# Performance work log

Measured on AMD Instinct MI355X. Metric: run time of the kernel, lower is better.

Reference implementation:

```python
import jax, jax.numpy as jnp
from jax import lax
import numpy as np

T, B, I = 512, 64, 1024
L, H = 2, 1024

def setup_inputs() -> dict:
    key = jax.random.key(0)
    k1, k2, k3 = jax.random.split(key, 3)
    scale = 1.0 / np.sqrt(H)
    return {
        "x": jax.random.normal(k1, (T, B, I), dtype=jnp.float32),
        "w_ih": jax.random.normal(k2, (L, 4 * H, I), dtype=jnp.float32) * scale,
        "w_hh": jax.random.normal(k3, (L, 4 * H, H), dtype=jnp.float32) * scale,
        "b_ih": jnp.zeros((L, 4 * H), dtype=jnp.float32),
        "b_hh": jnp.zeros((L, 4 * H), dtype=jnp.float32),
    }

def _lstm_layer(seq, wi, wh, b):
    # seq: [T, B, D]; wi: [4H, D]; wh: [4H, H]; b: [4H]
    Bsz = seq.shape[1]
    Hh = wh.shape[1]
    # precompute input projection for all timesteps (one big GEMM)
    xin = jnp.einsum('tbd,gd->tbg', seq, wi) + b  # [T, B, 4H]
    def step(carry, xt):
        h, c = carry
        gates = xt + h @ wh.T  # [B, 4H]
        i, f, g, o = jnp.split(gates, 4, axis=1)
        c = jax.nn.sigmoid(f) * c + jax.nn.sigmoid(i) * jnp.tanh(g)
        h = jax.nn.sigmoid(o) * jnp.tanh(c)
        return (h, c), h
    h0 = jnp.zeros((Bsz, Hh), seq.dtype)
    c0 = jnp.zeros((Bsz, Hh), seq.dtype)
    (hn, cn), out = lax.scan(step, (h0, c0), xin)
    return out, hn, cn

def reference(x, w_ih, w_hh, b_ih, b_hh):
    seq = x
    h_n, c_n = [], []
    for l in range(w_hh.shape[0]):
        seq, hn, cn = _lstm_layer(seq, w_ih[l], w_hh[l], b_ih[l] + b_hh[l])
        h_n.append(hn)
        c_n.append(cn)
    return seq, jnp.stack(h_n, 0), jnp.stack(c_n, 0)
```

## Files before the change

kernel.cpp:

```cpp
#include <hip/hip_runtime.h>
#include <cstddef>
#include <cstdint>

#define T_LEN   512
#define BATCH   64
#define IN_DIM  1024
#define HID     1024
#define GATES   4096
#define NLAYERS 2
#define BH      (BATCH * HID)
#define RBLK    256

typedef __bf16 bf16;
typedef __bf16 bf16x8 __attribute__((ext_vector_type(8)));
typedef float  f32x4  __attribute__((ext_vector_type(4)));

__global__ __launch_bounds__(256) void cvt_bf16(const float* __restrict__ in,
                                                bf16* __restrict__ out, int n4) {
    int i = blockIdx.x * blockDim.x + threadIdx.x;
    if (i >= n4) return;
    float4 v = ((const float4*)in)[i];
    bf16 o[4] = {(bf16)v.x, (bf16)v.y, (bf16)v.z, (bf16)v.w};
    *(uint2*)(out + 4 * (size_t)i) = *(uint2*)o;
}

__global__ __launch_bounds__(256) void lstm_layer(
    const bf16*  __restrict__ wi,
    const bf16*  __restrict__ wh,
    const float* __restrict__ bih,
    const float* __restrict__ bhh,
    const bf16*  __restrict__ xbf,
    bf16*        __restrict__ hseq,
    float*       __restrict__ outf,
    float*       __restrict__ hf32,
    float*       __restrict__ cbuf,
    unsigned*    __restrict__ bar)
{
    __shared__ bf16  Bi[16 * 1032];
    __shared__ bf16  Bh[16 * 1032];
    __shared__ float sg[4 * 272];

    const int bk   = blockIdx.x;
    const int j0   = bk * 4;
    const int tid  = threadIdx.x;
    const int lane = tid & 63;
    const int wv   = tid >> 6;
    const int m0   = wv * 16;
    const int quad = lane >> 4;
    const int l16  = lane & 15;

    unsigned* flags   = bar;
    unsigned* release = bar + 384;

    #pragma unroll
    for (int i = 0; i < 8; ++i) {
        int flat = i * 256 + tid;
        int row  = flat >> 7;
        int k16  = flat & 127;
        int grr  = (row >> 2) * 1024 + j0 + (row & 3);
        *(uint4*)&Bi[row * 1032 + k16 * 8] =
            *(const uint4*)(wi + (size_t)grr * IN_DIM + k16 * 8);
        *(uint4*)&Bh[row * 1032 + k16 * 8] =
            *(const uint4*)(wh + (size_t)grr * HID + k16 * 8);
    }

    const int cb = m0 + l16;
    const int cu = j0 + quad;
    float c = 0.f;

    const int gr = (l16 >> 2) * 1024 + j0 + (l16 & 3);
    const int bb = m0 + quad * 4;
    const float bias = bih[gr] + bhh[gr];

    __syncthreads();

    const bf16*  bibase = &Bi[l16 * 1032 + quad * 8];
    const bf16*  bhbase = &Bh[l16 * 1032 + quad * 8];
    const size_t arow   = (size_t)(m0 + l16) * HID + quad * 8;

    f32x4 acc0, acc1, acc2, acc3;
    {
        const bf16* xp = xbf + arow;
        acc0 = {bias, bias, bias, bias};
        acc1 = {0.f, 0.f, 0.f, 0.f};
        acc2 = {0.f, 0.f, 0.f, 0.f};
        acc3 = {0.f, 0.f, 0.f, 0.f};
        #pragma unroll
        for (int q = 0; q < 8; ++q) {
            const int k0 = q * 32;
            acc0 = __builtin_amdgcn_mfma_f32_16x16x32_bf16(
                *(const bf16x8*)(xp + k0),       *(const bf16x8*)(bibase + k0),       acc0, 0, 0, 0);
            acc1 = __builtin_amdgcn_mfma_f32_16x16x32_bf16(
                *(const bf16x8*)(xp + 256 + k0), *(const bf16x8*)(bibase + 256 + k0), acc1, 0, 0, 0);
            acc2 = __builtin_amdgcn_mfma_f32_16x16x32_bf16(
                *(const bf16x8*)(xp + 512 + k0), *(const bf16x8*)(bibase + 512 + k0), acc2, 0, 0, 0);
            acc3 = __builtin_amdgcn_mfma_f32_16x16x32_bf16(
                *(const bf16x8*)(xp + 768 + k0), *(const bf16x8*)(bibase + 768 + k0), acc3, 0, 0, 0);
        }
    }

    for (int tt = 0; tt < T_LEN; ++tt) {
        if (tt > 0) {
            const unsigned ep = (unsigned)tt;
            if (tid == 0) {
                unsigned guard = 0;
                while (__hip_atomic_load(release, __ATOMIC_RELAXED,
                                         __HIP_MEMORY_SCOPE_AGENT) < ep) {
                    __builtin_amdgcn_s_sleep(1);
                    if (++guard > (1u << 16)) break;
                }
            }
            __syncthreads();
            const bf16* hp = hseq + (size_t)(tt - 1) * BH + arow;
            #pragma unroll
            for (int q = 0; q < 8; ++q) {
                const int k0 = q * 32;
                acc0 = __builtin_amdgcn_mfma_f32_16x16x32_bf16(
                    *(const bf16x8*)(hp + k0),       *(const bf16x8*)(bhbase + k0),       acc0, 0, 0, 0);
                acc1 = __builtin_amdgcn_mfma_f32_16x16x32_bf16(
                    *(const bf16x8*)(hp + 256 + k0), *(const bf16x8*)(bhbase + 256 + k0), acc1, 0, 0, 0);
                acc2 = __builtin_amdgcn_mfma_f32_16x16x32_bf16(
                    *(const bf16x8*)(hp + 512 + k0), *(const bf16x8*)(bhbase + 512 + k0), acc2, 0, 0, 0);
                acc3 = __builtin_amdgcn_mfma_f32_16x16x32_bf16(
                    *(const bf16x8*)(hp + 768 + k0), *(const bf16x8*)(bhbase + 768 + k0), acc3, 0, 0, 0);
            }
        }

        f32x4 g4 = (acc0 + acc1) + (acc2 + acc3);

        #pragma unroll
        for (int r = 0; r < 4; ++r)
            sg[wv * 272 + (quad * 4 + r) * 17 + l16] = g4[r];
        const float* gp = &sg[wv * 272 + l16 * 17];
        float gi = gp[quad], gf = gp[4 + quad], gg = gp[8 + quad], go = gp[12 + quad];

        float si  = 1.f / (1.f + expf(-gi));
        float sf_ = 1.f / (1.f + expf(-gf));
        float so  = 1.f / (1.f + expf(-go));
        float cv  = sf_ * c + si * tanhf(gg);
        float hv  = so * tanhf(cv);
        c = cv;

        const size_t idx = (size_t)cb * HID + cu;
        float hvn = __shfl_xor(hv, 16);
        if ((quad & 1) == 0) {
            bf16 hb  = (bf16)hv;
            bf16 hbn = (bf16)hvn;
            unsigned pk = (unsigned)__builtin_bit_cast(unsigned short, hb) |
                          ((unsigned)__builtin_bit_cast(unsigned short, hbn) << 16);
            __hip_atomic_store((unsigned*)(hseq + (size_t)tt * BH + idx), pk,
                               __ATOMIC_RELAXED, __HIP_MEMORY_SCOPE_AGENT);
        }
        if (outf) outf[(size_t)tt * BH + idx] = hv;
        if (tt == T_LEN - 1) hf32[idx] = hv;

        if (tt != T_LEN - 1) {
            const unsigned ep = (unsigned)(tt + 1);
            asm volatile("s_waitcnt vmcnt(0)" ::: "memory");
            __syncthreads();
            if (tid == 0)
                __hip_atomic_store(flags + bk, ep,
                                   __ATOMIC_RELAXED, __HIP_MEMORY_SCOPE_AGENT);

            const bf16* xp = xbf + (size_t)(tt + 1) * BH + arow;
            acc0 = {bias, bias, bias, bias};
            acc1 = {0.f, 0.f, 0.f, 0.f};
            acc2 = {0.f, 0.f, 0.f, 0.f};
            acc3 = {0.f, 0.f, 0.f, 0.f};
            #pragma unroll
            for (int q = 0; q < 8; ++q) {
                const int k0 = q * 32;
                acc0 = __builtin_amdgcn_mfma_f32_16x16x32_bf16(
                    *(const bf16x8*)(xp + k0),       *(const bf16x8*)(bibase + k0),       acc0, 0, 0, 0);
                acc1 = __builtin_amdgcn_mfma_f32_16x16x32_bf16(
                    *(const bf16x8*)(xp + 256 + k0), *(const bf16x8*)(bibase + 256 + k0), acc1, 0, 0, 0);
                acc2 = __builtin_amdgcn_mfma_f32_16x16x32_bf16(
                    *(const bf16x8*)(xp + 512 + k0), *(const bf16x8*)(bibase + 512 + k0), acc2, 0, 0, 0);
                acc3 = __builtin_amdgcn_mfma_f32_16x16x32_bf16(
                    *(const bf16x8*)(xp + 768 + k0), *(const bf16x8*)(bibase + 768 + k0), acc3, 0, 0, 0);
            }

            if (bk == 0 && tid < 64) {
                unsigned guard = 0;
                for (;;) {
                    unsigned f0 = __hip_atomic_load(flags + tid,
                                   __ATOMIC_RELAXED, __HIP_MEMORY_SCOPE_AGENT);
                    unsigned f1 = __hip_atomic_load(flags + 64 + tid,
                                   __ATOMIC_RELAXED, __HIP_MEMORY_SCOPE_AGENT);
                    unsigned f2 = __hip_atomic_load(flags + 128 + tid,
                                   __ATOMIC_RELAXED, __HIP_MEMORY_SCOPE_AGENT);
                    unsigned f3 = __hip_atomic_load(flags + 192 + tid,
                                   __ATOMIC_RELAXED, __HIP_MEMORY_SCOPE_AGENT);
                    if (__all(f0 >= ep && f1 >= ep && f2 >= ep && f3 >= ep)) break;
                    __builtin_amdgcn_s_sleep(1);
                    if (++guard > (1u << 16)) break;
                }
                if (tid == 0)
                    __hip_atomic_store(release, ep,
                                       __ATOMIC_RELAXED, __HIP_MEMORY_SCOPE_AGENT);
            }
        }
    }

    cbuf[(size_t)cb * HID + cu] = c;
}

extern "C" void kernel_launch(void* const* d_in, const int* in_sizes, int n_in,
                              void* d_out, int out_size, void* d_ws, size_t ws_size,
                              hipStream_t stream) {
    const float* x    = (const float*)d_in[0];
    const float* w_ih = (const float*)d_in[1];
    const float* w_hh = (const float*)d_in[2];
    const float* b_ih = (const float*)d_in[3];
    const float* b_hh = (const float*)d_in[4];
    float* out = (float*)d_out;

    float* cbuf = (float*)d_ws;
    float* hf32 = cbuf + (size_t)BATCH * HID;
    bf16* seq1bf = (bf16*)(hf32 + (size_t)BATCH * HID);
    bf16* xh0    = seq1bf + (size_t)T_LEN * BATCH * HID;
    bf16* wibf   = xh0 + (size_t)T_LEN * BATCH * HID;
    bf16* whbf   = wibf + (size_t)GATES * IN_DIM;
    unsigned* bar = (unsigned*)(whbf + (size_t)GATES * HID);

    const size_t seqE = (size_t)T_LEN * BATCH * HID;
    const size_t BHs  = (size_t)BATCH * HID;

    cvt_bf16<<<(int)(seqE / 4 + 255) / 256, 256, 0, stream>>>(x, xh0, (int)(seqE / 4));

    for (int l = 0; l < NLAYERS; ++l) {
        const float* wi = w_ih + (size_t)l * GATES * IN_DIM;
        const float* wh = w_hh + (size_t)l * GATES * HID;
        const float* bi = b_ih + (size_t)l * GATES;
        const float* bh = b_hh + (size_t)l * GATES;

        cvt_bf16<<<(GATES * IN_DIM / 4 + 255) / 256, 256, 0, stream>>>(wi, wibf, GATES * IN_DIM / 4);
        cvt_bf16<<<(GATES * HID / 4 + 255) / 256, 256, 0, stream>>>(wh, whbf, GATES * HID / 4);

        hipMemsetAsync(bar, 0, 512 * sizeof(unsigned), stream);

        const bf16* xin_l = (l == 0) ? xh0 : seq1bf;
        bf16*       hseq  = (l == 0) ? seq1bf : xh0;
        float*      outf  = (l == 1) ? out : nullptr;

        const bf16*  wic = wibf;  const bf16* whc = whbf;
        const float* bic = bi;    const float* bhc = bh;
        float* hfc = hf32;  float* cbc = cbuf;  unsigned* barc = bar;
        void* args[10] = { (void*)&wic, (void*)&whc, (void*)&bic, (void*)&bhc,
                           (void*)&xin_l, (void*)&hseq, (void*)&outf,
                           (void*)&hfc, (void*)&cbc, (void*)&barc };
        hipLaunchCooperativeKernel((void*)lstm_layer, dim3(RBLK), dim3(256),
                                   args, 0, stream);

        hipMemcpyAsync(out + seqE + (size_t)l * BHs, hf32, BHs * sizeof(float),
                       hipMemcpyDeviceToDevice, stream);
        hipMemcpyAsync(out + seqE + (size_t)(NLAYERS + l) * BHs, cbuf, BHs * sizeof(float),
                       hipMemcpyDeviceToDevice, stream);
    }
}
```

Baseline: 10.15 ms.

## Pipeline both LSTM layers in one cooperative kernel with wavefront schedule

Replaces the two sequential per-layer cooperative launches with a single 512-block launch. Blocks 0-255 run layer 0 and blocks 256-511 run layer 1, with layer 1 lagging one timestep and sharing a grid barrier. This targets the serial latency of running 2x512 recurrent steps back to back by overlapping the layers into 513 barrier steps. In exchange, layer-1 steps do the input projection inside the critical path, the barrier now polls 512 flags, and the design depends on 512 blocks being co-resident.

```diff
diff --git a/kernel.cpp b/kernel.cpp
--- a/kernel.cpp
+++ b/kernel.cpp
@@ -9,7 +9,8 @@
 #define GATES   4096
 #define NLAYERS 2
 #define BH      (BATCH * HID)
-#define RBLK    256
+#define LBLK    256
+#define NBLK    512
 
 typedef __bf16 bf16;
 typedef __bf16 bf16x8 __attribute__((ext_vector_type(8)));
@@ -24,16 +25,35 @@
     *(uint2*)(out + 4 * (size_t)i) = *(uint2*)o;
 }
 
-__global__ __launch_bounds__(256) void lstm_layer(
-    const bf16*  __restrict__ wi,
-    const bf16*  __restrict__ wh,
+#define GEMV8(XP, BB)                                                          \
+    _Pragma("unroll")                                                          \
+    for (int q = 0; q < 8; ++q) {                                              \
+        const int k0 = q * 32;                                                 \
+        acc0 = __builtin_amdgcn_mfma_f32_16x16x32_bf16(                        \
+            *(const bf16x8*)((XP) + k0),       *(const bf16x8*)((BB) + k0),       acc0, 0, 0, 0); \
+        acc1 = __builtin_amdgcn_mfma_f32_16x16x32_bf16(                        \
+            *(const bf16x8*)((XP) + 256 + k0), *(const bf16x8*)((BB) + 256 + k0), acc1, 0, 0, 0); \
+        acc2 = __builtin_amdgcn_mfma_f32_16x16x32_bf16(                        \
+            *(const bf16x8*)((XP) + 512 + k0), *(const bf16x8*)((BB) + 512 + k0), acc2, 0, 0, 0); \
+        acc3 = __builtin_amdgcn_mfma_f32_16x16x32_bf16(                        \
+            *(const bf16x8*)((XP) + 768 + k0), *(const bf16x8*)((BB) + 768 + k0), acc3, 0, 0, 0); \
+    }
+
+__global__ __launch_bounds__(256) void lstm_pipe(
+    const bf16*  __restrict__ wi0,
+    const bf16*  __restrict__ wh0,
+    const bf16*  __restrict__ wi1,
+    const bf16*  __restrict__ wh1,
     const float* __restrict__ bih,
     const float* __restrict__ bhh,
     const bf16*  __restrict__ xbf,
-    bf16*        __restrict__ hseq,
+    bf16*        __restrict__ h0seq,
+    bf16*        __restrict__ h1seq,
     float*       __restrict__ outf,
-    float*       __restrict__ hf32,
-    float*       __restrict__ cbuf,
+    float*       __restrict__ hf0,
+    float*       __restrict__ hf1,
+    float*       __restrict__ cb0,
+    float*       __restrict__ cb1,
     unsigned*    __restrict__ bar)
 {
     __shared__ bf16  Bi[16 * 1032];
@@ -41,7 +61,9 @@
     __shared__ float sg[4 * 272];
 
     const int bk   = blockIdx.x;
-    const int j0   = bk * 4;
+    const bool isL1 = (bk >= LBLK);
+    const int lk   = bk & (LBLK - 1);
+    const int j0   = lk * 4;
     const int tid  = threadIdx.x;
     const int lane = tid & 63;
     const int wv   = tid >> 6;
@@ -50,7 +72,14 @@
     const int l16  = lane & 15;
 
     unsigned* flags   = bar;
-    unsigned* release = bar + 384;
+    unsigned* release = bar + 768;
+
+    const bf16* wiL = isL1 ? wi1 : wi0;
+    const bf16* whL = isL1 ? wh1 : wh0;
+    const int   boff = isL1 ? GATES : 0;
+    bf16*       hW  = isL1 ? h1seq : h0seq;
+    float*      hfL = isL1 ? hf1 : hf0;
+    float*      cbL = isL1 ? cb1 : cb0;
 
     #pragma unroll
     for (int i = 0; i < 8; ++i) {
@@ -59,9 +88,9 @@
         int k16  = flat & 127;
         int grr  = (row >> 2) * 1024 + j0 + (row & 3);
         *(uint4*)&Bi[row * 1032 + k16 * 8] =
-            *(const uint4*)(wi + (size_t)grr * IN_DIM + k16 * 8);
+            *(const uint4*)(wiL + (size_t)grr * IN_DIM + k16 * 8);
         *(uint4*)&Bh[row * 1032 + k16 * 8] =
-            *(const uint4*)(wh + (size_t)grr * HID + k16 * 8);
+            *(const uint4*)(whL + (size_t)grr * HID + k16 * 8);
     }
 
     const int cb = m0 + l16;
@@ -69,8 +98,7 @@
     float c = 0.f;
 
     const int gr = (l16 >> 2) * 1024 + j0 + (l16 & 3);
-    const int bb = m0 + quad * 4;
-    const float bias = bih[gr] + bhh[gr];
+    const float bias = bih[boff + gr] + bhh[boff + gr];
 
     __syncthreads();
 
@@ -79,29 +107,18 @@
     const size_t arow   = (size_t)(m0 + l16) * HID + quad * 8;
 
     f32x4 acc0, acc1, acc2, acc3;
-    {
+    if (!isL1) {
         const bf16* xp = xbf + arow;
         acc0 = {bias, bias, bias, bias};
         acc1 = {0.f, 0.f, 0.f, 0.f};
         acc2 = {0.f, 0.f, 0.f, 0.f};
         acc3 = {0.f, 0.f, 0.f, 0.f};
-        #pragma unroll
-        for (int q = 0; q < 8; ++q) {
-            const int k0 = q * 32;
-            acc0 = __builtin_amdgcn_mfma_f32_16x16x32_bf16(
-                *(const bf16x8*)(xp + k0),       *(const bf16x8*)(bibase + k0),       acc0, 0, 0, 0);
-            acc1 = __builtin_amdgcn_mfma_f32_16x16x32_bf16(
-                *(const bf16x8*)(xp + 256 + k0), *(const bf16x8*)(bibase + 256 + k0), acc1, 0, 0, 0);
-            acc2 = __builtin_amdgcn_mfma_f32_16x16x32_bf16(
-                *(const bf16x8*)(xp + 512 + k0), *(const bf16x8*)(bibase + 512 + k0), acc2, 0, 0, 0);
-            acc3 = __builtin_amdgcn_mfma_f32_16x16x32_bf16(
-                *(const bf16x8*)(xp + 768 + k0), *(const bf16x8*)(bibase + 768 + k0), acc3, 0, 0, 0);
-        }
-    }
-
-    for (int tt = 0; tt < T_LEN; ++tt) {
-        if (tt > 0) {
-            const unsigned ep = (unsigned)tt;
+        GEMV8(xp, bibase)
+    }
+
+    for (int s = 0; s < T_LEN + 1; ++s) {
+        if (s > 0) {
+            const unsigned ep = (unsigned)s;
             if (tid == 0) {
                 unsigned guard = 0;
                 while (__hip_atomic_load(release, __ATOMIC_RELAXED,
@@ -111,87 +128,86 @@
                 }
             }
             __syncthreads();
-            const bf16* hp = hseq + (size_t)(tt - 1) * BH + arow;
+        }
+
+        const bool active = isL1 ? (s >= 1) : (s < T_LEN);
+        if (active) {
+            const int t = isL1 ? (s - 1) : s;
+            if (isL1) {
+                const bf16* xp = h0seq + (size_t)t * BH + arow;
+                acc0 = {bias, bias, bias, bias};
+                acc1 = {0.f, 0.f, 0.f, 0.f};
+                acc2 = {0.f, 0.f, 0.f, 0.f};
+                acc3 = {0.f, 0.f, 0.f, 0.f};
+                GEMV8(xp, bibase)
+                if (t > 0) {
+                    const bf16* hp = h1seq + (size_t)(t - 1) * BH + arow;
+                    GEMV8(hp, bhbase)
+                }
+            } else {
+                if (t > 0) {
+                    const bf16* hp = h0seq + (size_t)(t - 1) * BH + arow;
+                    GEMV8(hp, bhbase)
+                }
+            }
+
+            f32x4 g4 = (acc0 + acc1) + (acc2 + acc3);
+
             #pragma unroll
-            for (int q = 0; q < 8; ++q) {
-                const int k0 = q * 32;
-                acc0 = __builtin_amdgcn_mfma_f32_16x16x32_bf16(
-                    *(const bf16x8*)(hp + k0),       *(const bf16x8*)(bhbase + k0),       acc0, 0, 0, 0);
-                acc1 = __builtin_amdgcn_mfma_f32_16x16x32_bf16(
-                    *(const bf16x8*)(hp + 256 + k0), *(const bf16x8*)(bhbase + 256 + k0), acc1, 0, 0, 0);
-                acc2 = __builtin_amdgcn_mfma_f32_16x16x32_bf16(
-                    *(const bf16x8*)(hp + 512 + k0), *(const bf16x8*)(bhbase + 512 + k0), acc2, 0, 0, 0);
-                acc3 = __builtin_amdgcn_mfma_f32_16x16x32_bf16(
-                    *(const bf16x8*)(hp + 768 + k0), *(const bf16x8*)(bhbase + 768 + k0), acc3, 0, 0, 0);
-            }
+            for (int r = 0; r < 4; ++r)
+                sg[wv * 272 + (quad * 4 + r) * 17 + l16] = g4[r];
+            const float* gp = &sg[wv * 272 + l16 * 17];
+            float gi = gp[quad], gf = gp[4 + quad], gg = gp[8 + quad], go = gp[12 + quad];
+
+            float si  = 1.f / (1.f + expf(-gi));
+            float sf_ = 1.f / (1.f + expf(-gf));
+            float so  = 1.f / (1.f + expf(-go));
+            float cv  = sf_ * c + si * tanhf(gg);
+            float hv  = so * tanhf(cv);
+            c = cv;
+
+            const size_t idx = (size_t)cb * HID + cu;
+            float hvn = __shfl_xor(hv, 16);
+            if ((quad & 1) == 0) {
+                bf16 hb  = (bf16)hv;
+                bf16 hbn = (bf16)hvn;
+                unsigned pk = (unsigned)__builtin_bit_cast(unsigned short, hb) |
+                              ((unsigned)__builtin_bit_cast(unsigned short, hbn) << 16);
+                __hip_atomic_store((unsigned*)(hW + (size_t)t * BH + idx), pk,
+                                   __ATOMIC_RELAXED, __HIP_MEMORY_SCOPE_AGENT);
+            }
+            if (isL1) outf[(size_t)t * BH + idx] = hv;
+            if (t == T_LEN - 1) hfL[idx] = hv;
         }
 
-        f32x4 g4 = (acc0 + acc1) + (acc2 + acc3);
-
-        #pragma unroll
-        for (int r = 0; r < 4; ++r)
-            sg[wv * 272 + (quad * 4 + r) * 17 + l16] = g4[r];
-        const float* gp = &sg[wv * 272 + l16 * 17];
-        float gi = gp[quad], gf = gp[4 + quad], gg = gp[8 + quad], go = gp[12 + quad];
-
-        float si  = 1.f / (1.f + expf(-gi));
-        float sf_ = 1.f / (1.f + expf(-gf));
-        float so  = 1.f / (1.f + expf(-go));
-        float cv  = sf_ * c + si * tanhf(gg);
-        float hv  = so * tanhf(cv);
-        c = cv;
-
-        const size_t idx = (size_t)cb * HID + cu;
-        float hvn = __shfl_xor(hv, 16);
-        if ((quad & 1) == 0) {
-            bf16 hb  = (bf16)hv;
-            bf16 hbn = (bf16)hvn;
-            unsigned pk = (unsigned)__builtin_bit_cast(unsigned short, hb) |
-                          ((unsigned)__builtin_bit_cast(unsigned short, hbn) << 16);
-            __hip_atomic_store((unsigned*)(hseq + (size_t)tt * BH + idx), pk,
-                               __ATOMIC_RELAXED, __HIP_MEMORY_SCOPE_AGENT);
-        }
-        if (outf) outf[(size_t)tt * BH + idx] = hv;
-        if (tt == T_LEN - 1) hf32[idx] = hv;
-
-        if (tt != T_LEN - 1) {
-            const unsigned ep = (unsigned)(tt + 1);
+        if (s < T_LEN) {
+            const unsigned ep = (unsigned)(s + 1);
             asm volatile("s_waitcnt vmcnt(0)" ::: "memory");
             __syncthreads();
             if (tid == 0)
                 __hip_atomic_store(flags + bk, ep,
                                    __ATOMIC_RELAXED, __HIP_MEMORY_SCOPE_AGENT);
 
-            const bf16* xp = xbf + (size_t)(tt + 1) * BH + arow;
-            acc0 = {bias, bias, bias, bias};
-            acc1 = {0.f, 0.f, 0.f, 0.f};
-            acc2 = {0.f, 0.f, 0.f, 0.f};
-            acc3 = {0.f, 0.f, 0.f, 0.f};
-            #pragma unroll
-            for (int q = 0; q < 8; ++q) {
-                const int k0 = q * 32;
-                acc0 = __builtin_amdgcn_mfma_f32_16x16x32_bf16(
-                    *(const bf16x8*)(xp + k0),       *(const bf16x8*)(bibase + k0),       acc0, 0, 0, 0);
-                acc1 = __builtin_amdgcn_mfma_f32_16x16x32_bf16(
-                    *(const bf16x8*)(xp + 256 + k0), *(const bf16x8*)(bibase + 256 + k0), acc1, 0, 0, 0);
-                acc2 = __builtin_amdgcn_mfma_f32_16x16x32_bf16(
-                    *(const bf16x8*)(xp + 512 + k0), *(const bf16x8*)(bibase + 512 + k0), acc2, 0, 0, 0);
-                acc3 = __builtin_amdgcn_mfma_f32_16x16x32_bf16(
-                    *(const bf16x8*)(xp + 768 + k0), *(const bf16x8*)(bibase + 768 + k0), acc3, 0, 0, 0);
-            }
-
-            if (bk == 0 && tid < 64) {
+            if (!isL1 && s < T_LEN - 1) {
+                const bf16* xp = xbf + (size_t)(s + 1) * BH + arow;
+                acc0 = {bias, bias, bias, bias};
+                acc1 = {0.f, 0.f, 0.f, 0.f};
+                acc2 = {0.f, 0.f, 0.f, 0.f};
+                acc3 = {0.f, 0.f, 0.f, 0.f};
+                GEMV8(xp, bibase)
+            }
+
+            if (bk == NBLK - 1 && tid < 64) {
                 unsigned guard = 0;
                 for (;;) {
-                    unsigned f0 = __hip_atomic_load(flags + tid,
-                                   __ATOMIC_RELAXED, __HIP_MEMORY_SCOPE_AGENT);
-                    unsigned f1 = __hip_atomic_load(flags + 64 + tid,
-                                   __ATOMIC_RELAXED, __HIP_MEMORY_SCOPE_AGENT);
-                    unsigned f2 = __hip_atomic_load(flags + 128 + tid,
-                                   __ATOMIC_RELAXED, __HIP_MEMORY_SCOPE_AGENT);
-                    unsigned f3 = __hip_atomic_load(flags + 192 + tid,
-                                   __ATOMIC_RELAXED, __HIP_MEMORY_SCOPE_AGENT);
-                    if (__all(f0 >= ep && f1 >= ep && f2 >= ep && f3 >= ep)) break;
+                    bool good = true;
+                    #pragma unroll
+                    for (int j = 0; j < 8; ++j) {
+                        unsigned f = __hip_atomic_load(flags + tid + 64 * j,
+                                       __ATOMIC_RELAXED, __HIP_MEMORY_SCOPE_AGENT);
+                        good = good && (f >= ep);
+                    }
+                    if (__all(good)) break;
                     __builtin_amdgcn_s_sleep(1);
                     if (++guard > (1u << 16)) break;
                 }
@@ -202,7 +218,7 @@
         }
     }
 
-    cbuf[(size_t)cb * HID + cu] = c;
+    cbL[(size_t)cb * HID + cu] = c;
 }
 
 extern "C" void kernel_launch(void* const* d_in, const int* in_sizes, int n_in,
@@ -215,46 +231,48 @@
     const float* b_hh = (const float*)d_in[4];
     float* out = (float*)d_out;
 
-    float* cbuf = (float*)d_ws;
-    float* hf32 = cbuf + (size_t)BATCH * HID;
-    bf16* seq1bf = (bf16*)(hf32 + (size_t)BATCH * HID);
-    bf16* xh0    = seq1bf + (size_t)T_LEN * BATCH * HID;
-    bf16* wibf   = xh0 + (size_t)T_LEN * BATCH * HID;
-    bf16* whbf   = wibf + (size_t)GATES * IN_DIM;
-    unsigned* bar = (unsigned*)(whbf + (size_t)GATES * HID);
-
     const size_t seqE = (size_t)T_LEN * BATCH * HID;
     const size_t BHs  = (size_t)BATCH * HID;
 
-    cvt_bf16<<<(int)(seqE / 4 + 255) / 256, 256, 0, stream>>>(x, xh0, (int)(seqE / 4));
-
-    for (int l = 0; l < NLAYERS; ++l) {
-        const float* wi = w_ih + (size_t)l * GATES * IN_DIM;
-        const float* wh = w_hh + (size_t)l * GATES * HID;
-        const float* bi = b_ih + (size_t)l * GATES;
-        const float* bh = b_hh + (size_t)l * GATES;
-
-        cvt_bf16<<<(GATES * IN_DIM / 4 + 255) / 256, 256, 0, stream>>>(wi, wibf, GATES * IN_DIM / 4);
-        cvt_bf16<<<(GATES * HID / 4 + 255) / 256, 256, 0, stream>>>(wh, whbf, GATES * HID / 4);
-
-        hipMemsetAsync(bar, 0, 512 * sizeof(unsigned), stream);
-
-        const bf16* xin_l = (l == 0) ? xh0 : seq1bf;
-        bf16*       hseq  = (l == 0) ? seq1bf : xh0;
-        float*      outf  = (l == 1) ? out : nullptr;
-
-        const bf16*  wic = wibf;  const bf16* whc = whbf;
-        const float* bic = bi;    const float* bhc = bh;
-        float* hfc = hf32;  float* cbc = cbuf;  unsigned* barc = bar;
-        void* args[10] = { (void*)&wic, (void*)&whc, (void*)&bic, (void*)&bhc,
-                           (void*)&xin_l, (void*)&hseq, (void*)&outf,
-                           (void*)&hfc, (void*)&cbc, (void*)&barc };
-        hipLaunchCooperativeKernel((void*)lstm_layer, dim3(RBLK), dim3(256),
-                                   args, 0, stream);
-
-        hipMemcpyAsync(out + seqE + (size_t)l * BHs, hf32, BHs * sizeof(float),
-                       hipMemcpyDeviceToDevice, stream);
-        hipMemcpyAsync(out + seqE + (size_t)(NLAYERS + l) * BHs, cbuf, BHs * sizeof(float),
-                       hipMemcpyDeviceToDevice, stream);
-    }
+    bf16* xbf   = (bf16*)d_ws;
+    bf16* h0seq = xbf + seqE;
+    bf16* h1seq = h0seq + seqE;
+    bf16* wi0b  = h1seq + seqE;
+    bf16* wh0b  = wi0b + (size_t)GATES * IN_DIM;
+    bf16* wi1b  = wh0b + (size_t)GATES * HID;
+    bf16* wh1b  = wi1b + (size_t)GATES * HID;
+    float* hf0  = (float*)(wh1b + (size_t)GATES * HID);
+    float* hf1  = hf0 + BHs;
+    float* cb0  = hf1 + BHs;
+    float* cb1  = cb0 + BHs;
+    unsigned* bar = (unsigned*)(cb1 + BHs);
+
+    cvt_bf16<<<(int)(seqE / 4 + 255) / 256, 256, 0, stream>>>(x, xbf, (int)(seqE / 4));
+    cvt_bf16<<<(GATES * IN_DIM / 4 + 255) / 256, 256, 0, stream>>>(
+        w_ih, wi0b, GATES * IN_DIM / 4);
+    cvt_bf16<<<(GATES * HID / 4 + 255) / 256, 256, 0, stream>>>(
+        w_hh, wh0b, GATES * HID / 4);
+    cvt_bf16<<<(GATES * HID / 4 + 255) / 256, 256, 0, stream>>>(
+        w_ih + (size_t)GATES * IN_DIM, wi1b, GATES * HID / 4);
+    cvt_bf16<<<(GATES * HID / 4 + 255) / 256, 256, 0, stream>>>(
+        w_hh + (size_t)GATES * HID, wh1b, GATES * HID / 4);
+
+    hipMemsetAsync(bar, 0, 1024 * sizeof(unsigned), stream);
+
+    void* args[15] = { (void*)&wi0b, (void*)&wh0b, (void*)&wi1b, (void*)&wh1b,
+                       (void*)&b_ih, (void*)&b_hh, (void*)&xbf,
+                       (void*)&h0seq, (void*)&h1seq, (void*)&out,
+                       (void*)&hf0, (void*)&hf1, (void*)&cb0, (void*)&cb1,
+                       (void*)&bar };
+    hipLaunchCooperativeKernel((void*)lstm_pipe, dim3(NBLK), dim3(256),
+                               args, 0, stream);
+
+    hipMemcpyAsync(out + seqE,           hf0, BHs * sizeof(float),
+                   hipMemcpyDeviceToDevice, stream);
+    hipMemcpyAsync(out + seqE + BHs,     hf1, BHs * sizeof(float),
+                   hipMemcpyDeviceToDevice, stream);
+    hipMemcpyAsync(out + seqE + 2 * BHs, cb0, BHs * sizeof(float),
+                   hipMemcpyDeviceToDevice, stream);
+    hipMemcpyAsync(out + seqE + 3 * BHs, cb1, BHs * sizeof(float),
+                   hipMemcpyDeviceToDevice, stream);
 }
```

New measurement: 9.228 ms. 1.1x faster.
